# Kernel tuning notes

Measured on AMD Instinct MI355X. Metric: run time of the kernel, lower is better.

Reference implementation:

```python
import jax, jax.numpy as jnp
from jax import lax
import numpy as np

LN_EPS = 1e-5

def layernorm(x, g, b):
    m = jnp.mean(x, axis=-1, keepdims=True)
    v = jnp.mean((x - m) ** 2, axis=-1, keepdims=True)
    return (x - m) / jnp.sqrt(v + LN_EPS) * g + b

def setup_inputs() -> dict:
    key = jax.random.key(0)
    ks = jax.random.split(key, 16)
    B, C, T = 64, 8, 2048
    K, L = 128, 64
    E, NC = 64, 10
    s = 0.05
    d = {}
    d["x"] = jax.random.normal(ks[0], (B, C, T), jnp.float32)
    d["shapelets"] = jax.random.uniform(ks[1], (K, C, L), jnp.float32, -1.0, 1.0)
    # local encoder: Linear(K->E) + LayerNorm
    d["w_loc"] = jax.random.normal(ks[2], (K, E), jnp.float32) * s
    d["b_loc"] = jnp.zeros((E,), jnp.float32)
    d["g_loc"] = jnp.ones((E,), jnp.float32)
    d["be_loc"] = jnp.zeros((E,), jnp.float32)
    # global conv: Conv2d(1->16,(3,5)) , Conv2d(16->32,(3,5))
    d["conv1_w"] = jax.random.normal(ks[3], (16, 1, 3, 5), jnp.float32) * s
    d["conv1_b"] = jnp.zeros((16,), jnp.float32)
    d["conv2_w"] = jax.random.normal(ks[4], (32, 16, 3, 5), jnp.float32) * s
    d["conv2_b"] = jnp.zeros((32,), jnp.float32)
    # global encoder: Linear(32->E) + LayerNorm
    d["w_glob"] = jax.random.normal(ks[5], (32, E), jnp.float32) * s
    d["b_glob"] = jnp.zeros((E,), jnp.float32)
    d["g_glob"] = jnp.ones((E,), jnp.float32)
    d["be_glob"] = jnp.zeros((E,), jnp.float32)
    # MultiheadAttention (torch layout): in_proj (3E,E), out_proj (E,E)
    d["in_proj_w"] = jax.random.normal(ks[6], (3 * E, E), jnp.float32) * s
    d["in_proj_b"] = jnp.zeros((3 * E,), jnp.float32)
    d["out_w"] = jax.random.normal(ks[7], (E, E), jnp.float32) * s
    d["out_b"] = jnp.zeros((E,), jnp.float32)
    # MLP head: Linear(E->E//2), Linear(E//2->NC)
    d["mlp_w1"] = jax.random.normal(ks[8], (E, E // 2), jnp.float32) * s
    d["mlp_b1"] = jnp.zeros((E // 2,), jnp.float32)
    d["mlp_w2"] = jax.random.normal(ks[9], (E // 2, NC), jnp.float32) * s
    d["mlp_b2"] = jnp.zeros((NC,), jnp.float32)
    return d

def reference(x, shapelets, w_loc, b_loc, g_loc, be_loc,
              conv1_w, conv1_b, conv2_w, conv2_b,
              w_glob, b_glob, g_glob, be_glob,
              in_proj_w, in_proj_b, out_w, out_b,
              mlp_w1, mlp_b1, mlp_w2, mlp_b2):
    B, C, T = x.shape
    K, _, L = shapelets.shape
    n_heads = 8
    # ---- shapelet min squared distance via ||w||^2 - 2*corr + ||s||^2 ----
    # corr: (B, K, W) with W = T - L + 1; same math as the unfold/broadcast version
    corr = lax.conv_general_dilated(x, shapelets, (1,), 'VALID',
                                    dimension_numbers=('NCH', 'OIH', 'NCH'))
    win_sq = lax.conv_general_dilated(x * x, jnp.ones((1, C, L), x.dtype), (1,), 'VALID',
                                      dimension_numbers=('NCH', 'OIH', 'NCH'))  # (B,1,W)
    s_sq = jnp.sum(shapelets * shapelets, axis=(1, 2))  # (K,)
    dist_sq = win_sq - 2.0 * corr + s_sq[None, :, None]  # (B,K,W)
    feat = jnp.min(dist_sq, axis=2)  # (B,K)
    # ---- local encoder ----
    local = layernorm(jax.nn.relu(feat @ w_loc + b_loc), g_loc, be_loc)  # (B,E)
    # ---- global conv branch on (B,1,C,T) ----
    h = x[:, None, :, :]
    h = lax.conv_general_dilated(h, conv1_w, (1, 1), [(1, 1), (2, 2)],
                                 dimension_numbers=('NCHW', 'OIHW', 'NCHW'))
    h = jax.nn.relu(h + conv1_b[None, :, None, None])
    h = lax.reduce_window(h, -jnp.inf, lax.max, (1, 1, 1, 2), (1, 1, 1, 2), 'VALID')
    h = lax.conv_general_dilated(h, conv2_w, (1, 1), [(1, 1), (2, 2)],
                                 dimension_numbers=('NCHW', 'OIHW', 'NCHW'))
    h = jax.nn.relu(h + conv2_b[None, :, None, None])
    h = lax.reduce_window(h, -jnp.inf, lax.max, (1, 1, 1, 2), (1, 1, 1, 2), 'VALID')
    g = jnp.mean(h, axis=(2, 3))  # AdaptiveAvgPool2d((1,1)) + Flatten -> (B,32)
    glob = layernorm(jax.nn.relu(g @ w_glob + b_glob), g_glob, be_glob)  # (B,E)
    # ---- cross attention (query len 1, kv len 1) ----
    E = local.shape[-1]
    hd = E // n_heads
    wq, wk, wv = jnp.split(in_proj_w, 3, axis=0)
    bq, bk, bv = jnp.split(in_proj_b, 3)
    q = (local @ wq.T + bq).reshape(B, n_heads, hd)
    k = (glob @ wk.T + bk).reshape(B, n_heads, hd)
    v = (glob @ wv.T + bv).reshape(B, n_heads, hd)
    scores = jnp.sum(q * k, axis=-1, keepdims=True) / jnp.sqrt(jnp.float32(hd))  # (B,H,1)
    attn = jax.nn.softmax(scores, axis=-1)  # kv length 1 -> all ones
    attn_out = (attn * v).reshape(B, E) @ out_w.T + out_b  # (B,E)
    # ---- MLP head (dropout is identity in eval) ----
    hmid = jax.nn.relu(attn_out @ mlp_w1 + mlp_b1)
    return hmid @ mlp_w2 + mlp_b2
```

## Files before the change

### kernel.cpp

```cpp
#include <hip/hip_runtime.h>
#include <math.h>


typedef __attribute__((ext_vector_type(4))) _Float16 f16x4;
typedef __attribute__((ext_vector_type(8)))  _Float16 f16x8;
typedef __attribute__((ext_vector_type(16))) float    f32x16;

#define WT 64
#define NT 16
#define H1_OFF   0
#define XS_OFF   21760
#define LDS_BYTES 26368

template <int CTRL>
__device__ __forceinline__ float dppf(float v) {
    return __uint_as_float(__builtin_amdgcn_update_dpp(
        0u, __float_as_uint(v), CTRL, 0xF, 0xF, true));
}
#define DPP_XOR1 0xB1
#define DPP_XOR2 0x4E
#define DPP_ROR4 0x124
#define DPP_ROR8 0x128

__global__ void prep_frags(const float* __restrict__ w2, _Float16* __restrict__ fragg) {
    const int t    = blockIdx.x;
    const int lane = threadIdx.x;
    const int kh   = t / 5, kw = t - kh * 5;
    const int oc   = lane & 31;
    const int ic0  = (lane >> 5) * 8;
    f16x8 hv;
    #pragma unroll
    for (int j = 0; j < 8; ++j)
        hv[j] = (_Float16)w2[((oc * 16 + ic0 + j) * 3 + kh) * 5 + kw];
    *(f16x8*)&fragg[(t * 64 + lane) * 8] = hv;
}

__global__ __launch_bounds__(256, 4) void conv_fused(
    const float* __restrict__ x,
    const float* __restrict__ w1, const float* __restrict__ b1,
    const float* __restrict__ b2,
    const _Float16* __restrict__ fragg,
    float* __restrict__ part)
{
    const int wt  = blockIdx.x;
    const int b   = blockIdx.y;
    const int tid = threadIdx.x;
    const int w0  = wt * WT;

    __shared__ __align__(16) unsigned int ldsu[LDS_BYTES / 4];
    _Float16* h1 = (_Float16*)((char*)ldsu + H1_OFF);
    float*    xs = (float*)((char*)ldsu + XS_OFF);

    const int q = tid & 3;
    float wreg[60];
    float bias1[4];
    #pragma unroll
    for (int j = 0; j < 4; ++j) {
        #pragma unroll
        for (int k = 0; k < 15; ++k) wreg[j * 15 + k] = w1[(q * 4 + j) * 15 + k];
        bias1[j] = b1[q * 4 + j];
    }

    const int t0 = 2 * w0 - 6;
    for (int i = tid; i < 8 * 144; i += 256) {
        int r = i / 144, tl = i - r * 144;
        int t = t0 + tl;
        float v = 0.f;
        if (tl < 140 && t >= 0 && t < 2048) v = x[(b * 8 + r) * 2048 + t];
        xs[i] = v;
    }
    {
        unsigned int* hh = (unsigned int*)h1;
        for (int i = tid; i < 544; i += 256) {
            hh[i] = 0u; hh[4896 + i] = 0u;
        }
    }
    __syncthreads();

    #pragma unroll
    for (int pass = 0; pass < 3; ++pass) {
        if (pass == 2 && tid >= 32) break;
        const int idx = (tid >> 2) + pass * 64;
        const int r   = idx / 17;
        const int c4  = idx - r * 17;
        const int cb  = c4 * 8;
        float xv[3][12];
        #pragma unroll
        for (int pq = 0; pq < 3; ++pq) {
            int rr = r + pq - 1;
            if (rr >= 0 && rr < 8) {
                const float4* p = (const float4*)&xs[rr * 144 + cb];
                float4 a0 = p[0], a1 = p[1], a2 = p[2];
                xv[pq][0]=a0.x; xv[pq][1]=a0.y; xv[pq][2]=a0.z; xv[pq][3]=a0.w;
                xv[pq][4]=a1.x; xv[pq][5]=a1.y; xv[pq][6]=a1.z; xv[pq][7]=a1.w;
                xv[pq][8]=a2.x; xv[pq][9]=a2.y; xv[pq][10]=a2.z; xv[pq][11]=a2.w;
            } else {
                #pragma unroll
                for (int z = 0; z < 12; ++z) xv[pq][z] = 0.f;
            }
        }
        #pragma unroll
        for (int cc = 0; cc < 4; ++cc) {
            const int wc = w0 - 2 + 4 * c4 + cc;
            f16x4 hv;
            #pragma unroll
            for (int j = 0; j < 4; ++j) {
                float c0 = bias1[j], c1 = bias1[j];
                #pragma unroll
                for (int kh = 0; kh < 3; ++kh)
                    #pragma unroll
                    for (int kw = 0; kw < 5; ++kw) {
                        float wgt = wreg[j * 15 + kh * 5 + kw];
                        c0 = fmaf(xv[kh][2 * cc + kw],     wgt, c0);
                        c1 = fmaf(xv[kh][2 * cc + kw + 1], wgt, c1);
                    }
                float v = fmaxf(fmaxf(c0, c1), 0.f);
                if (wc < 0 || wc >= 1024) v = 0.f;
                hv[j] = (_Float16)v;
            }
            *(f16x4*)&h1[((r + 1) * 68 + 4 * c4 + cc) * 16 + q * 4] = hv;
        }
    }
    __syncthreads();

    const int lane  = tid & 63;
    const int wave  = tid >> 6;
    const int laneN = lane & 31;
    const int icoff = (lane >> 5) * 8;
    const int half  = lane >> 5;

    f32x16 acc[4];
    #pragma unroll
    for (int nt = 0; nt < 4; ++nt)
        #pragma unroll
        for (int r = 0; r < 16; ++r) acc[nt][r] = 0.f;

    const f16x8* Ag = (const f16x8*)fragg;
    f16x8 a_cur = Ag[lane];
    for (int t = 0; t < 15; ++t) {
        f16x8 a_nxt = (t < 14) ? Ag[(t + 1) * 64 + lane] : a_cur;
        int kh = t / 5, kw = t - kh * 5;
        #pragma unroll
        for (int nt = 0; nt < 4; ++nt) {
            int hrow = 2 * wave + (nt >> 1);
            int wn0  = (nt & 1) * 32;
            int idx  = ((hrow + kh) * 68 + wn0 + laneN + kw) * 16 + icoff;
            f16x8 bv = *(const f16x8*)&h1[idx];
            acc[nt] = __builtin_amdgcn_mfma_f32_32x32x16_f16(a_cur, bv, acc[nt], 0, 0, 0);
        }
        a_cur = a_nxt;
    }

    float b2v[16], sums[16];
    #pragma unroll
    for (int r = 0; r < 16; ++r) {
        b2v[r]  = b2[(r & 3) + 8 * (r >> 2) + 4 * half];
        sums[r] = 0.f;
    }
    #pragma unroll
    for (int nt = 0; nt < 4; ++nt)
        #pragma unroll
        for (int r = 0; r < 16; ++r) {
            float d = acc[nt][r] + b2v[r];
            float o = fmaxf(fmaxf(d, dppf<DPP_XOR1>(d)), 0.f);
            sums[r] += o;
        }
    #pragma unroll
    for (int r = 0; r < 16; ++r) {
        float s = sums[r];
        s += dppf<DPP_XOR1>(s);
        s += dppf<DPP_XOR2>(s);
        s += dppf<DPP_ROR4>(s);
        s += dppf<DPP_ROR8>(s);
        sums[r] = s;
    }
    if ((lane & 15) == 0) {
        const int nh = (lane >> 4) & 1;
        #pragma unroll
        for (int r = 0; r < 16; ++r) {
            int oc = (r & 3) + 8 * (r >> 2) + 4 * half;
            part[((b * 32 + oc) * 16 + wt) * 8 + wave * 2 + nh] = 0.5f * sums[r];
        }
    }
}

__global__ void tail_kernel(
    const float* __restrict__ part,
    const float* __restrict__ w_glob, const float* __restrict__ b_glob,
    const float* __restrict__ g_glob, const float* __restrict__ be_glob,
    const float* __restrict__ in_proj_w, const float* __restrict__ in_proj_b,
    const float* __restrict__ out_w, const float* __restrict__ out_b,
    const float* __restrict__ mlp_w1, const float* __restrict__ mlp_b1,
    const float* __restrict__ mlp_w2, const float* __restrict__ mlp_b2,
    float* __restrict__ out)
{
    const int b = blockIdx.x;
    const int e = threadIdx.x;
    __shared__ float gs[32], glob_s[64], vs[64], aos[64], hms[32];

    if (e < 32) {
        float sm = 0.f;
        #pragma unroll
        for (int t = 0; t < 128; ++t) sm += part[(b * 32 + e) * 128 + t];
        gs[e] = sm * (1.f / 4096.f);
    }
    __syncthreads();

    float acc = b_glob[e];
    #pragma unroll
    for (int i = 0; i < 32; ++i) acc = fmaf(gs[i], w_glob[i * 64 + e], acc);
    acc = fmaxf(acc, 0.f);

    float m = acc;
    #pragma unroll
    for (int k = 32; k >= 1; k >>= 1) m += __shfl_xor(m, k);
    m *= (1.f / 64.f);
    float d = acc - m;
    float vv = d * d;
    #pragma unroll
    for (int k = 32; k >= 1; k >>= 1) vv += __shfl_xor(vv, k);
    vv *= (1.f / 64.f);
    float gl = d * (1.f / sqrtf(vv + 1e-5f)) * g_glob[e] + be_glob[e];
    glob_s[e] = gl;
    __syncthreads();

    float vval = in_proj_b[128 + e];
    #pragma unroll
    for (int j = 0; j < 64; ++j) vval = fmaf(glob_s[j], in_proj_w[(128 + e) * 64 + j], vval);
    vs[e] = vval;
    __syncthreads();

    float ao = out_b[e];
    #pragma unroll
    for (int j = 0; j < 64; ++j) ao = fmaf(vs[j], out_w[e * 64 + j], ao);
    aos[e] = ao;
    __syncthreads();

    if (e < 32) {
        float hm = mlp_b1[e];
        #pragma unroll
        for (int j = 0; j < 64; ++j) hm = fmaf(aos[j], mlp_w1[j * 32 + e], hm);
        hms[e] = fmaxf(hm, 0.f);
    }
    __syncthreads();

    if (e < 10) {
        float o = mlp_b2[e];
        #pragma unroll
        for (int i = 0; i < 32; ++i) o = fmaf(hms[i], mlp_w2[i * 10 + e], o);
        out[b * 10 + e] = o;
    }
}

extern "C" void kernel_launch(void* const* d_in, const int* in_sizes, int n_in,
                              void* d_out, int out_size, void* d_ws, size_t ws_size,
                              hipStream_t stream) {
    const float* x        = (const float*)d_in[0];
    const float* conv1_w  = (const float*)d_in[6];
    const float* conv1_b  = (const float*)d_in[7];
    const float* conv2_w  = (const float*)d_in[8];
    const float* conv2_b  = (const float*)d_in[9];
    const float* w_glob   = (const float*)d_in[10];
    const float* b_glob   = (const float*)d_in[11];
    const float* g_glob   = (const float*)d_in[12];
    const float* be_glob  = (const float*)d_in[13];
    const float* in_proj_w = (const float*)d_in[14];
    const float* in_proj_b = (const float*)d_in[15];
    const float* out_w    = (const float*)d_in[16];
    const float* out_b    = (const float*)d_in[17];
    const float* mlp_w1   = (const float*)d_in[18];
    const float* mlp_b1   = (const float*)d_in[19];
    const float* mlp_w2   = (const float*)d_in[20];
    const float* mlp_b2   = (const float*)d_in[21];

    _Float16* fragg = (_Float16*)d_ws;
    float* partials = (float*)((char*)d_ws + 15360);

    prep_frags<<<15, 64, 0, stream>>>(conv2_w, fragg);

    dim3 grid(NT, 64);
    conv_fused<<<grid, 256, 0, stream>>>(x, conv1_w, conv1_b, conv2_b, fragg, partials);

    tail_kernel<<<64, 64, 0, stream>>>(partials, w_glob, b_glob, g_glob, be_glob,
                                       in_proj_w, in_proj_b, out_w, out_b,
                                       mlp_w1, mlp_b1, mlp_w2, mlp_b2,
                                       (float*)d_out);
}
```

Measured before the change: 123.6 us.

## Split conv1 into a separate kernel writing fp16 activations to global memory

Conv1 (with its ReLU and max-pool) moves out of the fused conv kernel into its own kernel. Each block computes one full row for one batch element and writes the padded fp16 output to a global workspace. The conv2 kernel then loads its tile from that buffer instead of recomputing conv1 halo columns, and weight fragment prep is folded into the conv1 kernel to save one launch. This removes the redundant halo compute and the LDS staging of x, at the cost of a global round trip for the fp16 activations (about 16 MB).

```diff
diff --git a/kernel.cpp b/kernel.cpp
--- a/kernel.cpp
+++ b/kernel.cpp
@@ -6,11 +6,7 @@
 typedef __attribute__((ext_vector_type(8)))  _Float16 f16x8;
 typedef __attribute__((ext_vector_type(16))) float    f32x16;
 
-#define WT 64
-#define NT 16
-#define H1_OFF   0
-#define XS_OFF   21760
-#define LDS_BYTES 26368
+#define WPAD 1028
 
 template <int CTRL>
 __device__ __forceinline__ float dppf(float v) {
@@ -22,22 +18,92 @@
 #define DPP_ROR4 0x124
 #define DPP_ROR8 0x128
 
-__global__ void prep_frags(const float* __restrict__ w2, _Float16* __restrict__ fragg) {
-    const int t    = blockIdx.x;
-    const int lane = threadIdx.x;
-    const int kh   = t / 5, kw = t - kh * 5;
-    const int oc   = lane & 31;
-    const int ic0  = (lane >> 5) * 8;
-    f16x8 hv;
-    #pragma unroll
-    for (int j = 0; j < 8; ++j)
-        hv[j] = (_Float16)w2[((oc * 16 + ic0 + j) * 3 + kh) * 5 + kw];
-    *(f16x8*)&fragg[(t * 64 + lane) * 8] = hv;
-}
-
-__global__ __launch_bounds__(256, 4) void conv_fused(
+__global__ __launch_bounds__(256, 2) void conv1_kernel(
     const float* __restrict__ x,
     const float* __restrict__ w1, const float* __restrict__ b1,
+    const float* __restrict__ w2,
+    _Float16* __restrict__ fragg,
+    _Float16* __restrict__ h1g)
+{
+    const int blk = blockIdx.x;
+    const int b   = blk >> 3;
+    const int r   = blk & 7;
+    const int tid = threadIdx.x;
+
+    __shared__ __align__(16) float xrow[3][2056];
+
+    for (int i = tid; i < 3 * 2056; i += 256) {
+        int q = i / 2056, ci = i - q * 2056;
+        int c = ci - 2;
+        int rr = r + q - 1;
+        float v = 0.f;
+        if (rr >= 0 && rr < 8 && c >= 0 && c < 2048) v = x[(b * 8 + rr) * 2048 + c];
+        xrow[q][ci] = v;
+    }
+
+    if (blk < 15 && tid < 64) {
+        const int t = blk, lane = tid;
+        const int kh = t / 5, kw = t - kh * 5;
+        const int oc = lane & 31;
+        const int ic0 = (lane >> 5) * 8;
+        f16x8 hv;
+        #pragma unroll
+        for (int j = 0; j < 8; ++j)
+            hv[j] = (_Float16)w2[((oc * 16 + ic0 + j) * 3 + kh) * 5 + kw];
+        *(f16x8*)&fragg[(t * 64 + lane) * 8] = hv;
+    }
+    __syncthreads();
+
+    const int wp0 = tid * 4;
+    float xl[3][16];
+    #pragma unroll
+    for (int q = 0; q < 3; ++q) {
+        const float4* p = (const float4*)&xrow[q][8 * tid];
+        float4 a0 = p[0], a1 = p[1], a2 = p[2], a3 = p[3];
+        xl[q][0]=a0.x; xl[q][1]=a0.y; xl[q][2]=a0.z; xl[q][3]=a0.w;
+        xl[q][4]=a1.x; xl[q][5]=a1.y; xl[q][6]=a1.z; xl[q][7]=a1.w;
+        xl[q][8]=a2.x; xl[q][9]=a2.y; xl[q][10]=a2.z; xl[q][11]=a2.w;
+        xl[q][12]=a3.x; xl[q][13]=a3.y; xl[q][14]=a3.z; xl[q][15]=a3.w;
+    }
+
+    f16x8 o0[4], o1[4];
+    for (int ic = 0; ic < 16; ++ic) {
+        const float bb = b1[ic];
+        float wv[15];
+        #pragma unroll
+        for (int k = 0; k < 15; ++k) wv[k] = w1[ic * 15 + k];
+        #pragma unroll
+        for (int d = 0; d < 4; ++d) {
+            float c0 = bb, c1 = bb;
+            #pragma unroll
+            for (int kh = 0; kh < 3; ++kh)
+                #pragma unroll
+                for (int kw = 0; kw < 5; ++kw) {
+                    float w = wv[kh * 5 + kw];
+                    c0 = fmaf(xl[kh][2 * d + kw],     w, c0);
+                    c1 = fmaf(xl[kh][2 * d + kw + 1], w, c1);
+                }
+            float v = fmaxf(fmaxf(c0, c1), 0.f);
+            if (ic < 8) o0[d][ic] = (_Float16)v; else o1[d][ic - 8] = (_Float16)v;
+        }
+    }
+
+    _Float16* base = &h1g[(((size_t)b * 8 + r) * WPAD + wp0 + 2) * 16];
+    #pragma unroll
+    for (int d = 0; d < 4; ++d) {
+        *(f16x8*)&base[d * 16]     = o0[d];
+        *(f16x8*)&base[d * 16 + 8] = o1[d];
+    }
+    if (tid == 0 || tid == 255) {
+        _Float16* mb = &h1g[(((size_t)b * 8 + r) * WPAD + (tid ? 1026 : 0)) * 16];
+        f16x8 z = {};
+        *(f16x8*)&mb[0] = z; *(f16x8*)&mb[8] = z;
+        *(f16x8*)&mb[16] = z; *(f16x8*)&mb[24] = z;
+    }
+}
+
+__global__ __launch_bounds__(256, 4) void conv2_kernel(
+    const _Float16* __restrict__ h1g,
     const float* __restrict__ b2,
     const _Float16* __restrict__ fragg,
     float* __restrict__ part)
@@ -45,81 +111,20 @@
     const int wt  = blockIdx.x;
     const int b   = blockIdx.y;
     const int tid = threadIdx.x;
-    const int w0  = wt * WT;
-
-    __shared__ __align__(16) unsigned int ldsu[LDS_BYTES / 4];
-    _Float16* h1 = (_Float16*)((char*)ldsu + H1_OFF);
-    float*    xs = (float*)((char*)ldsu + XS_OFF);
-
-    const int q = tid & 3;
-    float wreg[60];
-    float bias1[4];
-    #pragma unroll
-    for (int j = 0; j < 4; ++j) {
-        #pragma unroll
-        for (int k = 0; k < 15; ++k) wreg[j * 15 + k] = w1[(q * 4 + j) * 15 + k];
-        bias1[j] = b1[q * 4 + j];
-    }
-
-    const int t0 = 2 * w0 - 6;
-    for (int i = tid; i < 8 * 144; i += 256) {
-        int r = i / 144, tl = i - r * 144;
-        int t = t0 + tl;
-        float v = 0.f;
-        if (tl < 140 && t >= 0 && t < 2048) v = x[(b * 8 + r) * 2048 + t];
-        xs[i] = v;
-    }
+    const int w0  = wt * 64;
+
+    __shared__ __align__(16) _Float16 h1[10 * 68 * 16];
+
     {
         unsigned int* hh = (unsigned int*)h1;
         for (int i = tid; i < 544; i += 256) {
-            hh[i] = 0u; hh[4896 + i] = 0u;
-        }
-    }
-    __syncthreads();
-
-    #pragma unroll
-    for (int pass = 0; pass < 3; ++pass) {
-        if (pass == 2 && tid >= 32) break;
-        const int idx = (tid >> 2) + pass * 64;
-        const int r   = idx / 17;
-        const int c4  = idx - r * 17;
-        const int cb  = c4 * 8;
-        float xv[3][12];
-        #pragma unroll
-        for (int pq = 0; pq < 3; ++pq) {
-            int rr = r + pq - 1;
-            if (rr >= 0 && rr < 8) {
-                const float4* p = (const float4*)&xs[rr * 144 + cb];
-                float4 a0 = p[0], a1 = p[1], a2 = p[2];
-                xv[pq][0]=a0.x; xv[pq][1]=a0.y; xv[pq][2]=a0.z; xv[pq][3]=a0.w;
-                xv[pq][4]=a1.x; xv[pq][5]=a1.y; xv[pq][6]=a1.z; xv[pq][7]=a1.w;
-                xv[pq][8]=a2.x; xv[pq][9]=a2.y; xv[pq][10]=a2.z; xv[pq][11]=a2.w;
-            } else {
-                #pragma unroll
-                for (int z = 0; z < 12; ++z) xv[pq][z] = 0.f;
-            }
-        }
-        #pragma unroll
-        for (int cc = 0; cc < 4; ++cc) {
-            const int wc = w0 - 2 + 4 * c4 + cc;
-            f16x4 hv;
-            #pragma unroll
-            for (int j = 0; j < 4; ++j) {
-                float c0 = bias1[j], c1 = bias1[j];
-                #pragma unroll
-                for (int kh = 0; kh < 3; ++kh)
-                    #pragma unroll
-                    for (int kw = 0; kw < 5; ++kw) {
-                        float wgt = wreg[j * 15 + kh * 5 + kw];
-                        c0 = fmaf(xv[kh][2 * cc + kw],     wgt, c0);
-                        c1 = fmaf(xv[kh][2 * cc + kw + 1], wgt, c1);
-                    }
-                float v = fmaxf(fmaxf(c0, c1), 0.f);
-                if (wc < 0 || wc >= 1024) v = 0.f;
-                hv[j] = (_Float16)v;
-            }
-            *(f16x4*)&h1[((r + 1) * 68 + 4 * c4 + cc) * 16 + q * 4] = hv;
-        }
+            hh[i] = 0u; hh[9 * 544 + i] = 0u;
+        }
+    }
+    for (int i = tid; i < 8 * 136; i += 256) {
+        int row = i / 136, ch = i - row * 136;
+        float4 v = *(const float4*)&h1g[(((size_t)b * 8 + row) * WPAD + w0) * 16 + ch * 8];
+        *(float4*)&h1[(row + 1) * 1088 + ch * 8] = v;
     }
     __syncthreads();
 
@@ -275,11 +280,12 @@
 
     _Float16* fragg = (_Float16*)d_ws;
     float* partials = (float*)((char*)d_ws + 15360);
-
-    prep_frags<<<15, 64, 0, stream>>>(conv2_w, fragg);
-
-    dim3 grid(NT, 64);
-    conv_fused<<<grid, 256, 0, stream>>>(x, conv1_w, conv1_b, conv2_b, fragg, partials);
+    _Float16* h1g   = (_Float16*)((char*)d_ws + 15360 + 1048576);
+
+    conv1_kernel<<<512, 256, 0, stream>>>(x, conv1_w, conv1_b, conv2_w, fragg, h1g);
+
+    dim3 grid(16, 64);
+    conv2_kernel<<<grid, 256, 0, stream>>>(h1g, conv2_b, fragg, partials);
 
     tail_kernel<<<64, 64, 0, stream>>>(partials, w_glob, b_glob, g_glob, be_glob,
                                        in_proj_w, in_proj_b, out_w, out_b,
```

Result: slower. 147.8 us (+19.6%).

## Fuse tail MLP into conv kernel using atomic accumulation and a grid counter

Applied to the files above, without the earlier changes.

Drops the separate tail kernel. Each conv block now reduces its per-channel sums in LDS and atomically adds them into a global per-batch accumulator, then bumps a global completion counter. The first 16 blocks spin until all 1024 blocks have finished and then run the global-encoder, attention and MLP head, one wave per batch. This is meant to remove the tail kernel's launch and the partial-buffer round trip. In exchange it adds a memset, float atomics that make the reduction order nondeterministic, and a spin-wait that assumes the blocks it waits on are resident or can still be scheduled.

```diff
diff --git a/kernel.cpp b/kernel.cpp
--- a/kernel.cpp
+++ b/kernel.cpp
@@ -6,11 +6,10 @@
 typedef __attribute__((ext_vector_type(8)))  _Float16 f16x8;
 typedef __attribute__((ext_vector_type(16))) float    f32x16;
 
-#define WT 64
-#define NT 16
 #define H1_OFF   0
 #define XS_OFF   21760
-#define LDS_BYTES 26368
+#define GS_OFF   26368
+#define LDS_BYTES 26496
 
 template <int CTRL>
 __device__ __forceinline__ float dppf(float v) {
@@ -40,16 +39,26 @@
     const float* __restrict__ w1, const float* __restrict__ b1,
     const float* __restrict__ b2,
     const _Float16* __restrict__ fragg,
-    float* __restrict__ part)
+    float* __restrict__ gacc,
+    int* __restrict__ cnt,
+    const float* __restrict__ w_glob, const float* __restrict__ b_glob,
+    const float* __restrict__ g_glob, const float* __restrict__ be_glob,
+    const float* __restrict__ in_proj_w, const float* __restrict__ in_proj_b,
+    const float* __restrict__ out_w, const float* __restrict__ out_b,
+    const float* __restrict__ mlp_w1, const float* __restrict__ mlp_b1,
+    const float* __restrict__ mlp_w2, const float* __restrict__ mlp_b2,
+    float* __restrict__ out)
 {
-    const int wt  = blockIdx.x;
-    const int b   = blockIdx.y;
-    const int tid = threadIdx.x;
-    const int w0  = wt * WT;
+    const int wt    = blockIdx.x;
+    const int b     = blockIdx.y;
+    const int linid = b * 16 + wt;
+    const int tid   = threadIdx.x;
+    const int w0    = wt * 64;
 
     __shared__ __align__(16) unsigned int ldsu[LDS_BYTES / 4];
-    _Float16* h1 = (_Float16*)((char*)ldsu + H1_OFF);
-    float*    xs = (float*)((char*)ldsu + XS_OFF);
+    _Float16* h1    = (_Float16*)((char*)ldsu + H1_OFF);
+    float*    xs    = (float*)((char*)ldsu + XS_OFF);
+    float*    gaccs = (float*)((char*)ldsu + GS_OFF);
 
     const int q = tid & 3;
     float wreg[60];
@@ -72,9 +81,10 @@
     {
         unsigned int* hh = (unsigned int*)h1;
         for (int i = tid; i < 544; i += 256) {
-            hh[i] = 0u; hh[4896 + i] = 0u;
-        }
-    }
+            hh[i] = 0u; hh[9 * 544 + i] = 0u;
+        }
+    }
+    if (tid < 32) gaccs[tid] = 0.f;
     __syncthreads();
 
     #pragma unroll
@@ -175,80 +185,80 @@
         sums[r] = s;
     }
     if ((lane & 15) == 0) {
-        const int nh = (lane >> 4) & 1;
         #pragma unroll
         for (int r = 0; r < 16; ++r) {
             int oc = (r & 3) + 8 * (r >> 2) + 4 * half;
-            part[((b * 32 + oc) * 16 + wt) * 8 + wave * 2 + nh] = 0.5f * sums[r];
-        }
-    }
-}
-
-__global__ void tail_kernel(
-    const float* __restrict__ part,
-    const float* __restrict__ w_glob, const float* __restrict__ b_glob,
-    const float* __restrict__ g_glob, const float* __restrict__ be_glob,
-    const float* __restrict__ in_proj_w, const float* __restrict__ in_proj_b,
-    const float* __restrict__ out_w, const float* __restrict__ out_b,
-    const float* __restrict__ mlp_w1, const float* __restrict__ mlp_b1,
-    const float* __restrict__ mlp_w2, const float* __restrict__ mlp_b2,
-    float* __restrict__ out)
-{
-    const int b = blockIdx.x;
-    const int e = threadIdx.x;
-    __shared__ float gs[32], glob_s[64], vs[64], aos[64], hms[32];
-
-    if (e < 32) {
-        float sm = 0.f;
-        #pragma unroll
-        for (int t = 0; t < 128; ++t) sm += part[(b * 32 + e) * 128 + t];
-        gs[e] = sm * (1.f / 4096.f);
+            atomicAdd(&gaccs[oc], sums[r]);
+        }
     }
     __syncthreads();
-
-    float acc = b_glob[e];
-    #pragma unroll
-    for (int i = 0; i < 32; ++i) acc = fmaf(gs[i], w_glob[i * 64 + e], acc);
-    acc = fmaxf(acc, 0.f);
-
-    float m = acc;
-    #pragma unroll
-    for (int k = 32; k >= 1; k >>= 1) m += __shfl_xor(m, k);
-    m *= (1.f / 64.f);
-    float d = acc - m;
-    float vv = d * d;
-    #pragma unroll
-    for (int k = 32; k >= 1; k >>= 1) vv += __shfl_xor(vv, k);
-    vv *= (1.f / 64.f);
-    float gl = d * (1.f / sqrtf(vv + 1e-5f)) * g_glob[e] + be_glob[e];
-    glob_s[e] = gl;
+    if (tid < 32) atomicAdd(&gacc[b * 32 + tid], 0.5f * gaccs[tid]);
     __syncthreads();
-
-    float vval = in_proj_b[128 + e];
-    #pragma unroll
-    for (int j = 0; j < 64; ++j) vval = fmaf(glob_s[j], in_proj_w[(128 + e) * 64 + j], vval);
-    vs[e] = vval;
-    __syncthreads();
-
-    float ao = out_b[e];
-    #pragma unroll
-    for (int j = 0; j < 64; ++j) ao = fmaf(vs[j], out_w[e * 64 + j], ao);
-    aos[e] = ao;
-    __syncthreads();
-
-    if (e < 32) {
-        float hm = mlp_b1[e];
-        #pragma unroll
-        for (int j = 0; j < 64; ++j) hm = fmaf(aos[j], mlp_w1[j * 32 + e], hm);
-        hms[e] = fmaxf(hm, 0.f);
-    }
-    __syncthreads();
-
-    if (e < 10) {
-        float o = mlp_b2[e];
-        #pragma unroll
-        for (int i = 0; i < 32; ++i) o = fmaf(hms[i], mlp_w2[i * 10 + e], o);
-        out[b * 10 + e] = o;
+    if (tid == 0) { __threadfence(); atomicAdd(cnt, 1); }
+
+    if (linid < 16) {
+        if (tid == 0) { while (atomicAdd(cnt, 0) < 1024) { } }
+        __syncthreads();
+        __threadfence();
+        const int bt = linid * 4 + wave;
+        float* tl     = (float*)ldsu + wave * 256;
+        float* gs     = tl;
+        float* glob_s = tl + 32;
+        float* vs     = tl + 96;
+        float* aos    = tl + 160;
+        float* hms    = tl + 224;
+
+        if (lane < 32) {
+            float gv = atomicAdd(&gacc[bt * 32 + lane], 0.0f);
+            gs[lane] = gv * (1.f / 4096.f);
+        }
+        __syncthreads();
+
+        float a2 = b_glob[lane];
+        #pragma unroll
+        for (int i = 0; i < 32; ++i) a2 = fmaf(gs[i], w_glob[i * 64 + lane], a2);
+        a2 = fmaxf(a2, 0.f);
+
+        float m = a2;
+        #pragma unroll
+        for (int k = 32; k >= 1; k >>= 1) m += __shfl_xor(m, k);
+        m *= (1.f / 64.f);
+        float d = a2 - m;
+        float vv = d * d;
+        #pragma unroll
+        for (int k = 32; k >= 1; k >>= 1) vv += __shfl_xor(vv, k);
+        vv *= (1.f / 64.f);
+        float gl = d * (1.f / sqrtf(vv + 1e-5f)) * g_glob[lane] + be_glob[lane];
+        glob_s[lane] = gl;
+        __syncthreads();
+
+        float vval = in_proj_b[128 + lane];
+        #pragma unroll
+        for (int j = 0; j < 64; ++j)
+            vval = fmaf(glob_s[j], in_proj_w[(128 + lane) * 64 + j], vval);
+        vs[lane] = vval;
+        __syncthreads();
+
+        float ao = out_b[lane];
+        #pragma unroll
+        for (int j = 0; j < 64; ++j) ao = fmaf(vs[j], out_w[lane * 64 + j], ao);
+        aos[lane] = ao;
+        __syncthreads();
+
+        if (lane < 32) {
+            float hm = mlp_b1[lane];
+            #pragma unroll
+            for (int j = 0; j < 64; ++j) hm = fmaf(aos[j], mlp_w1[j * 32 + lane], hm);
+            hms[lane] = fmaxf(hm, 0.f);
+        }
+        __syncthreads();
+
+        if (lane < 10) {
+            float o = mlp_b2[lane];
+            #pragma unroll
+            for (int i = 0; i < 32; ++i) o = fmaf(hms[i], mlp_w2[i * 10 + lane], o);
+            out[bt * 10 + lane] = o;
+        }
     }
 }
 
@@ -274,15 +284,18 @@
     const float* mlp_b2   = (const float*)d_in[21];
 
     _Float16* fragg = (_Float16*)d_ws;
-    float* partials = (float*)((char*)d_ws + 15360);
+    float* gacc     = (float*)((char*)d_ws + 15360);
+    int*   cnt      = (int*)((char*)d_ws + 15360 + 8192);
+
+    hipMemsetAsync((char*)d_ws + 15360, 0, 8192 + 4, stream);
 
     prep_frags<<<15, 64, 0, stream>>>(conv2_w, fragg);
 
-    dim3 grid(NT, 64);
-    conv_fused<<<grid, 256, 0, stream>>>(x, conv1_w, conv1_b, conv2_b, fragg, partials);
-
-    tail_kernel<<<64, 64, 0, stream>>>(partials, w_glob, b_glob, g_glob, be_glob,
-                                       in_proj_w, in_proj_b, out_w, out_b,
-                                       mlp_w1, mlp_b1, mlp_w2, mlp_b2,
-                                       (float*)d_out);
+    dim3 grid(16, 64);
+    conv_fused<<<grid, 256, 0, stream>>>(x, conv1_w, conv1_b, conv2_b, fragg,
+                                         gacc, cnt,
+                                         w_glob, b_glob, g_glob, be_glob,
+                                         in_proj_w, in_proj_b, out_w, out_b,
+                                         mlp_w1, mlp_b1, mlp_w2, mlp_b2,
+                                         (float*)d_out);
 }
```

Result: slower. 153.5 us (+24.2%).
